# Performance work log

Measured on AMD Instinct MI355X. Metric: run time of the kernel, lower is better.

Reference implementation:

```python
import jax, jax.numpy as jnp
import numpy as np

V, F = 100000, 200000
N, H, W, K = 4, 512, 512, 4
SIGMA = 1e-4
GAMMA = 1e-4
BG = (1.0, 1.0, 1.0)
EPS = 1e-10
ZNEAR, ZFAR = 1.0, 100.0


def setup_inputs() -> dict:
    key = jax.random.key(0)
    ks = jax.random.split(key, 7)
    verts = jax.random.normal(ks[0], (V, 3), dtype=jnp.float32)
    vn = jax.random.normal(ks[1], (V, 3), dtype=jnp.float32)
    vertex_normals = vn / jnp.maximum(jnp.linalg.norm(vn, axis=-1, keepdims=True), 1e-12)
    bc = jax.random.uniform(ks[2], (N, H, W, K, 3), dtype=jnp.float32) + 1e-3
    bary_coords = bc / jnp.sum(bc, axis=-1, keepdims=True)
    # signed pixel-to-face distances, small scale comparable to sigma
    dists = jax.random.normal(ks[3], (N, H, W, K), dtype=jnp.float32) * 1e-4
    zbuf = jax.random.uniform(ks[4], (N, H, W, K), minval=ZNEAR, maxval=ZFAR, dtype=jnp.float32)
    faces = jax.random.randint(ks[5], (F, 3), 0, V, dtype=jnp.int64 if jax.config.jax_enable_x64 else jnp.int32)
    # include -1 entries (empty pixels), as produced by the rasterizer
    pix_to_face = jax.random.randint(ks[6], (N, H, W, K), -1, F, dtype=jnp.int64 if jax.config.jax_enable_x64 else jnp.int32)
    return {"verts": verts, "vertex_normals": vertex_normals, "bary_coords": bary_coords,
            "dists": dists, "zbuf": zbuf, "faces": faces, "pix_to_face": pix_to_face}


def reference(verts, vertex_normals, bary_coords, dists, zbuf, faces, pix_to_face):
    dtype = bary_coords.dtype
    # --- NormalCalcuate: gather per-face vertex normals and interpolate ---
    faces_normals = vertex_normals[faces]                      # [F, 3, 3]
    valid = pix_to_face >= 0                                   # [N,H,W,K]
    idx = jnp.where(valid, pix_to_face, 0)
    attrs = faces_normals[idx]                                 # [N,H,W,K,3(verts),3(ch)]
    pixel_normals = jnp.einsum('nhwkv,nhwkvc->nhwkc', bary_coords, attrs)
    pixel_normals = jnp.where(valid[..., None], pixel_normals, jnp.zeros((), dtype))
    # --- softmax_rgb_blend (rgb part only) ---
    maskf = valid.astype(dtype)
    prob = jax.nn.sigmoid(-dists / SIGMA) * maskf              # coverage weights
    z_inv = (ZFAR - zbuf) / (ZFAR - ZNEAR) * maskf
    z_inv_max = jnp.maximum(jnp.max(z_inv, axis=-1, keepdims=True), EPS)
    w_num = prob * jnp.exp((z_inv - z_inv_max) / GAMMA)        # [N,H,W,K]
    delta = jnp.maximum(jnp.exp((EPS - z_inv_max) / GAMMA), EPS)  # [N,H,W,1]
    denom = jnp.sum(w_num, axis=-1, keepdims=True) + delta
    bg = jnp.asarray(BG, dtype)
    rgb = (jnp.einsum('nhwk,nhwkc->nhwc', w_num, pixel_normals) + delta * bg) / denom
    # --- F.normalize(dim=3) ---
    norm = jnp.maximum(jnp.linalg.norm(rgb, axis=-1, keepdims=True), 1e-12)
    return rgb / norm
```

## Files before the change

### kernel.cpp

```cpp
#include <hip/hip_runtime.h>
#include <hip/hip_bf16.h>

namespace {
constexpr int N_ = 4, H_ = 512, W_ = 512, K_ = 4;
constexpr int F_ = 200000;
constexpr float SIGMA_ = 1e-4f;
constexpr float GAMMA_ = 1e-4f;
constexpr float EPS_   = 1e-10f;
constexpr float ZNEAR_ = 1.0f, ZFAR_ = 100.0f;

constexpr int P_ = N_ * H_ * W_;
constexpr int SHADER_BLOCKS  = 1024;
constexpr int SHADER_THREADS = SHADER_BLOCKS * 256;
constexpr int ITERS = P_ / SHADER_THREADS;
static_assert(P_ % SHADER_THREADS == 0, "grid must tile P exactly");

typedef float        f32x4 __attribute__((ext_vector_type(4), aligned(4)));
typedef int          i32x4 __attribute__((ext_vector_type(4), aligned(4)));
typedef float        f32x3 __attribute__((ext_vector_type(3), aligned(4)));
typedef unsigned int u32x4 __attribute__((ext_vector_type(4), aligned(16)));

struct PixIn { i32x4 f4; f32x4 dv, zv, bA, bB, bC; };
}


__device__ __forceinline__ unsigned int oct_encode(float x, float y, float z) {
    const float inv = 1.0f / (fabsf(x) + fabsf(y) + fabsf(z));
    const float px = x * inv, py = y * inv, pz = z * inv;
    const float wx = (1.0f - fabsf(py)) * copysignf(1.0f, px);
    const float wy = (1.0f - fabsf(px)) * copysignf(1.0f, py);
    const bool neg = pz < 0.0f;
    const float ex = neg ? wx : px;
    const float ey = neg ? wy : py;
    const int ix = (int)rintf(ex * 32767.0f);
    const int iy = (int)rintf(ey * 32767.0f);
    return ((unsigned int)ix & 0xffffu) | (((unsigned int)iy & 0xffffu) << 16);
}

__device__ __forceinline__ void oct_decode_raw(unsigned int e,
                                               float& x, float& y, float& z,
                                               float& inv) {
    const float fx = (float)(short)(unsigned short)(e & 0xffffu) * (1.0f / 32767.0f);
    const float fy = (float)(short)(unsigned short)(e >> 16)     * (1.0f / 32767.0f);
    z = 1.0f - fabsf(fx) - fabsf(fy);
    const float t = fmaxf(-z, 0.0f);
    const float xx = fx - copysignf(t, fx);
    const float yy = fy - copysignf(t, fy);
    x = xx; y = yy;
    inv = rsqrtf(xx * xx + yy * yy + z * z);
}

__global__ __launch_bounds__(256) void build_fnorm_kernel(
    const float*  __restrict__ vnorm,
    const int*    __restrict__ faces,
    unsigned int* __restrict__ fnorm)
{
    const int f = blockIdx.x * blockDim.x + threadIdx.x;
    if (f >= F_) return;
    const i32x4 fv = *reinterpret_cast<const i32x4*>(faces + 3 * (size_t)f);
    const f32x4 n0 = *reinterpret_cast<const f32x4*>(vnorm + 3 * (size_t)fv.x);
    const f32x4 n1 = *reinterpret_cast<const f32x4*>(vnorm + 3 * (size_t)fv.y);
    const f32x4 n2 = *reinterpret_cast<const f32x4*>(vnorm + 3 * (size_t)fv.z);
    const unsigned long long e0 = oct_encode(n0.x, n0.y, n0.z);
    const unsigned long long e1 = oct_encode(n1.x, n1.y, n1.z);
    const unsigned long long e2 = oct_encode(n2.x, n2.y, n2.z);
    unsigned long long* dst =
        reinterpret_cast<unsigned long long*>(fnorm + (size_t)f * 4);
    __hip_atomic_store(dst + 0, e0 | (e1 << 32), __ATOMIC_RELAXED, __HIP_MEMORY_SCOPE_AGENT);
    __hip_atomic_store(dst + 1, e2,              __ATOMIC_RELAXED, __HIP_MEMORY_SCOPE_AGENT);
}

__device__ __forceinline__ PixIn load_pix(const int*   __restrict__ ptf,
                                          const float* __restrict__ dists,
                                          const float* __restrict__ zbuf,
                                          const float* __restrict__ bary,
                                          int p) {
    PixIn s;
    s.f4 = __builtin_nontemporal_load(reinterpret_cast<const i32x4*>(ptf) + p);
    s.dv = __builtin_nontemporal_load(reinterpret_cast<const f32x4*>(dists) + p);
    s.zv = __builtin_nontemporal_load(reinterpret_cast<const f32x4*>(zbuf) + p);
    const f32x4* bp = reinterpret_cast<const f32x4*>(bary + (size_t)p * 12);
    s.bA = __builtin_nontemporal_load(bp + 0);
    s.bB = __builtin_nontemporal_load(bp + 1);
    s.bC = __builtin_nontemporal_load(bp + 2);
    return s;
}

__global__ __launch_bounds__(256, 4) void normal_shader_kernel(
    const unsigned int* __restrict__ fnorm,
    const float*        __restrict__ bary,
    const float*        __restrict__ dists,
    const float*        __restrict__ zbuf,
    const int*          __restrict__ ptf,
    float*              __restrict__ out)
{
    const int tid = blockIdx.x * 256 + threadIdx.x;

    PixIn cur = load_pix(ptf, dists, zbuf, bary, tid);

#pragma unroll
    for (int it = 0; it < ITERS; ++it) {
        const int p = tid + it * SHADER_THREADS;
        const int fidx[4] = {cur.f4.x, cur.f4.y, cur.f4.z, cur.f4.w};

        u32x4 row[4];
#pragma unroll
        for (int k = 0; k < K_; ++k) {
            const int r = (fidx[k] < 0) ? 0 : fidx[k];
            row[k] = reinterpret_cast<const u32x4*>(fnorm)[r];
        }

        PixIn nxt = cur;
        if (it + 1 < ITERS)
            nxt = load_pix(ptf, dists, zbuf, bary, p + SHADER_THREADS);

        const float d[4] = {cur.dv.x, cur.dv.y, cur.dv.z, cur.dv.w};
        const float z[4] = {cur.zv.x, cur.zv.y, cur.zv.z, cur.zv.w};
        float prob[4], zinv[4], zmax = EPS_;
#pragma unroll
        for (int k = 0; k < K_; ++k) {
            const bool valid = fidx[k] >= 0;
            prob[k] = valid ? 1.0f / (1.0f + __expf(d[k] * (1.0f / SIGMA_))) : 0.0f;
            zinv[k] = valid ? (ZFAR_ - z[k]) * (1.0f / (ZFAR_ - ZNEAR_)) : 0.0f;
            zmax = fmaxf(zmax, zinv[k]);
        }
        const float delta = fmaxf(__expf((EPS_ - zmax) * (1.0f / GAMMA_)), EPS_);
        float wn[4];
#pragma unroll
        for (int k = 0; k < K_; ++k)
            wn[k] = prob[k] * __expf((zinv[k] - zmax) * (1.0f / GAMMA_));

        const float bb[12] = {cur.bA.x, cur.bA.y, cur.bA.z, cur.bA.w,
                              cur.bB.x, cur.bB.y, cur.bB.z, cur.bB.w,
                              cur.bC.x, cur.bC.y, cur.bC.z, cur.bC.w};
        float acc0 = 0.f, acc1 = 0.f, acc2 = 0.f, wsum = 0.f;
#pragma unroll
        for (int k = 0; k < K_; ++k) {
            const float w = wn[k];
            wsum += w;
            float x0, y0, z0, i0, x1, y1, z1, i1, x2, y2, z2, i2;
            oct_decode_raw(row[k].x, x0, y0, z0, i0);
            oct_decode_raw(row[k].y, x1, y1, z1, i1);
            oct_decode_raw(row[k].z, x2, y2, z2, i2);
            const float s0 = (w * bb[3 * k + 0]) * i0;
            const float s1 = (w * bb[3 * k + 1]) * i1;
            const float s2 = (w * bb[3 * k + 2]) * i2;
            acc0 += s0 * x0 + s1 * x1 + s2 * x2;
            acc1 += s0 * y0 + s1 * y1 + s2 * y2;
            acc2 += s0 * z0 + s1 * z1 + s2 * z2;
        }
        const float inv_denom = 1.0f / (wsum + delta);
        const float r0 = (acc0 + delta) * inv_denom;
        const float r1 = (acc1 + delta) * inv_denom;
        const float r2 = (acc2 + delta) * inv_denom;
        const float nrm = fmaxf(sqrtf(r0 * r0 + r1 * r1 + r2 * r2), 1e-12f);
        const float inv = 1.0f / nrm;
        __builtin_nontemporal_store(
            f32x3{r0 * inv, r1 * inv, r2 * inv},
            reinterpret_cast<f32x3*>(out + (size_t)p * 3));

        cur = nxt;
    }
}

__global__ __launch_bounds__(256) void normal_shader_fused_kernel(
    const float* __restrict__ vnorm,
    const float* __restrict__ bary,
    const float* __restrict__ dists,
    const float* __restrict__ zbuf,
    const int*   __restrict__ faces,
    const int*   __restrict__ ptf,
    float*       __restrict__ out,
    int P)
{
    const int p = blockIdx.x * blockDim.x + threadIdx.x;
    if (p >= P) return;
    const i32x4 f4 = reinterpret_cast<const i32x4*>(ptf)[p];
    const int fidx[4] = {f4.x, f4.y, f4.z, f4.w};
    const f32x4 dv = reinterpret_cast<const f32x4*>(dists)[p];
    const f32x4 zv = reinterpret_cast<const f32x4*>(zbuf)[p];
    const float d[4] = {dv.x, dv.y, dv.z, dv.w};
    const float z[4] = {zv.x, zv.y, zv.z, zv.w};
    float prob[4], zinv[4], zmax = EPS_;
#pragma unroll
    for (int k = 0; k < K_; ++k) {
        const bool valid = fidx[k] >= 0;
        prob[k] = valid ? 1.0f / (1.0f + __expf(d[k] * (1.0f / SIGMA_))) : 0.0f;
        zinv[k] = valid ? (ZFAR_ - z[k]) * (1.0f / (ZFAR_ - ZNEAR_)) : 0.0f;
        zmax = fmaxf(zmax, zinv[k]);
    }
    const float delta = fmaxf(__expf((EPS_ - zmax) * (1.0f / GAMMA_)), EPS_);
    float wn[4];
#pragma unroll
    for (int k = 0; k < K_; ++k) wn[k] = prob[k] * __expf((zinv[k] - zmax) * (1.0f / GAMMA_));
    int cl[4];
#pragma unroll
    for (int k = 0; k < K_; ++k) cl[k] = (fidx[k] < 0) ? 0 : fidx[k];
    i32x4 fv[4];
#pragma unroll
    for (int k = 0; k < K_; ++k) fv[k] = *reinterpret_cast<const i32x4*>(faces + 3 * (size_t)cl[k]);
    const f32x4* bp = reinterpret_cast<const f32x4*>(bary + (size_t)p * 12);
    const f32x4 bA = bp[0], bB = bp[1], bC = bp[2];
    const float bb[12] = {bA.x, bA.y, bA.z, bA.w, bB.x, bB.y, bB.z, bB.w, bC.x, bC.y, bC.z, bC.w};
    f32x4 n0[4], n1[4], n2[4];
#pragma unroll
    for (int k = 0; k < K_; ++k) {
        n0[k] = *reinterpret_cast<const f32x4*>(vnorm + 3 * (size_t)fv[k].x);
        n1[k] = *reinterpret_cast<const f32x4*>(vnorm + 3 * (size_t)fv[k].y);
        n2[k] = *reinterpret_cast<const f32x4*>(vnorm + 3 * (size_t)fv[k].z);
    }
    float acc0 = 0.f, acc1 = 0.f, acc2 = 0.f, wsum = 0.f;
#pragma unroll
    for (int k = 0; k < K_; ++k) {
        wsum += wn[k];
        const float b0 = bb[3 * k], b1 = bb[3 * k + 1], b2 = bb[3 * k + 2];
        acc0 += wn[k] * (b0 * n0[k].x + b1 * n1[k].x + b2 * n2[k].x);
        acc1 += wn[k] * (b0 * n0[k].y + b1 * n1[k].y + b2 * n2[k].y);
        acc2 += wn[k] * (b0 * n0[k].z + b1 * n1[k].z + b2 * n2[k].z);
    }
    const float inv_denom = 1.0f / (wsum + delta);
    const float r0 = (acc0 + delta) * inv_denom;
    const float r1 = (acc1 + delta) * inv_denom;
    const float r2 = (acc2 + delta) * inv_denom;
    const float nrm = fmaxf(sqrtf(r0 * r0 + r1 * r1 + r2 * r2), 1e-12f);
    const float inv = 1.0f / nrm;
    float* op = out + (size_t)p * 3;
    op[0] = r0 * inv; op[1] = r1 * inv; op[2] = r2 * inv;
}

extern "C" void kernel_launch(void* const* d_in, const int* in_sizes, int n_in,
                              void* d_out, int out_size, void* d_ws, size_t ws_size,
                              hipStream_t stream) {
    const float* vnorm = (const float*)d_in[1];
    const float* bary  = (const float*)d_in[2];
    const float* dists = (const float*)d_in[3];
    const float* zbuf  = (const float*)d_in[4];
    const int*   faces = (const int*)d_in[5];
    const int*   ptf   = (const int*)d_in[6];
    float*       out   = (float*)d_out;

    const int P = N_ * H_ * W_;
    const size_t table_bytes = (size_t)F_ * 16;

    if (ws_size >= table_bytes) {
        unsigned int* fnorm = (unsigned int*)d_ws;
        hipLaunchKernelGGL(build_fnorm_kernel,
                           dim3((F_ + 255) / 256), dim3(256), 0, stream,
                           vnorm, faces, fnorm);
        hipLaunchKernelGGL(normal_shader_kernel,
                           dim3(SHADER_BLOCKS), dim3(256), 0, stream,
                           fnorm, bary, dists, zbuf, ptf, out);
    } else {
        hipLaunchKernelGGL(normal_shader_fused_kernel,
                           dim3((P + 255) / 256), dim3(256), 0, stream,
                           vnorm, bary, dists, zbuf, faces, ptf, out, P);
    }
}
```

Baseline: 164.4 us.

## Use one thread per pixel and drop the software-pipelined persistent loop

Replaces the persistent-style shader, where 1024 blocks each loop over several pixels with next-iteration loads prefetched, with a plain grid of one thread per pixel. Occupancy and the hardware scheduler now hide memory latency instead of the manual double buffering, and the launch-bounds occupancy hint is removed. It also drops the per-component scale in the octahedral decode, since the later rsqrt normalisation cancels it. The trade-off is more blocks to launch and the loss of explicit prefetch overlap.

```diff
diff --git a/kernel.cpp b/kernel.cpp
--- a/kernel.cpp
+++ b/kernel.cpp
@@ -10,17 +10,13 @@
 constexpr float ZNEAR_ = 1.0f, ZFAR_ = 100.0f;
 
 constexpr int P_ = N_ * H_ * W_;
-constexpr int SHADER_BLOCKS  = 1024;
-constexpr int SHADER_THREADS = SHADER_BLOCKS * 256;
-constexpr int ITERS = P_ / SHADER_THREADS;
-static_assert(P_ % SHADER_THREADS == 0, "grid must tile P exactly");
+constexpr int SHADER_BLOCKS = P_ / 256;
+static_assert(P_ % 256 == 0, "grid must tile P exactly");
 
 typedef float        f32x4 __attribute__((ext_vector_type(4), aligned(4)));
 typedef int          i32x4 __attribute__((ext_vector_type(4), aligned(4)));
 typedef float        f32x3 __attribute__((ext_vector_type(3), aligned(4)));
 typedef unsigned int u32x4 __attribute__((ext_vector_type(4), aligned(16)));
-
-struct PixIn { i32x4 f4; f32x4 dv, zv, bA, bB, bC; };
 }
 
 
@@ -40,12 +36,12 @@
 __device__ __forceinline__ void oct_decode_raw(unsigned int e,
                                                float& x, float& y, float& z,
                                                float& inv) {
-    const float fx = (float)(short)(unsigned short)(e & 0xffffu) * (1.0f / 32767.0f);
-    const float fy = (float)(short)(unsigned short)(e >> 16)     * (1.0f / 32767.0f);
-    z = 1.0f - fabsf(fx) - fabsf(fy);
+    const float X = (float)(short)(unsigned short)(e & 0xffffu);
+    const float Y = (float)(short)(unsigned short)(e >> 16);
+    z = 32767.0f - fabsf(X) - fabsf(Y);
     const float t = fmaxf(-z, 0.0f);
-    const float xx = fx - copysignf(t, fx);
-    const float yy = fy - copysignf(t, fy);
+    const float xx = X - copysignf(t, X);
+    const float yy = Y - copysignf(t, Y);
     x = xx; y = yy;
     inv = rsqrtf(xx * xx + yy * yy + z * z);
 }
@@ -70,23 +66,7 @@
     __hip_atomic_store(dst + 1, e2,              __ATOMIC_RELAXED, __HIP_MEMORY_SCOPE_AGENT);
 }
 
-__device__ __forceinline__ PixIn load_pix(const int*   __restrict__ ptf,
-                                          const float* __restrict__ dists,
-                                          const float* __restrict__ zbuf,
-                                          const float* __restrict__ bary,
-                                          int p) {
-    PixIn s;
-    s.f4 = __builtin_nontemporal_load(reinterpret_cast<const i32x4*>(ptf) + p);
-    s.dv = __builtin_nontemporal_load(reinterpret_cast<const f32x4*>(dists) + p);
-    s.zv = __builtin_nontemporal_load(reinterpret_cast<const f32x4*>(zbuf) + p);
-    const f32x4* bp = reinterpret_cast<const f32x4*>(bary + (size_t)p * 12);
-    s.bA = __builtin_nontemporal_load(bp + 0);
-    s.bB = __builtin_nontemporal_load(bp + 1);
-    s.bC = __builtin_nontemporal_load(bp + 2);
-    return s;
-}
-
-__global__ __launch_bounds__(256, 4) void normal_shader_kernel(
+__global__ __launch_bounds__(256) void normal_shader_kernel(
     const unsigned int* __restrict__ fnorm,
     const float*        __restrict__ bary,
     const float*        __restrict__ dists,
@@ -94,73 +74,68 @@
     const int*          __restrict__ ptf,
     float*              __restrict__ out)
 {
-    const int tid = blockIdx.x * 256 + threadIdx.x;
-
-    PixIn cur = load_pix(ptf, dists, zbuf, bary, tid);
-
-#pragma unroll
-    for (int it = 0; it < ITERS; ++it) {
-        const int p = tid + it * SHADER_THREADS;
-        const int fidx[4] = {cur.f4.x, cur.f4.y, cur.f4.z, cur.f4.w};
-
-        u32x4 row[4];
-#pragma unroll
-        for (int k = 0; k < K_; ++k) {
-            const int r = (fidx[k] < 0) ? 0 : fidx[k];
-            row[k] = reinterpret_cast<const u32x4*>(fnorm)[r];
-        }
-
-        PixIn nxt = cur;
-        if (it + 1 < ITERS)
-            nxt = load_pix(ptf, dists, zbuf, bary, p + SHADER_THREADS);
-
-        const float d[4] = {cur.dv.x, cur.dv.y, cur.dv.z, cur.dv.w};
-        const float z[4] = {cur.zv.x, cur.zv.y, cur.zv.z, cur.zv.w};
-        float prob[4], zinv[4], zmax = EPS_;
-#pragma unroll
-        for (int k = 0; k < K_; ++k) {
-            const bool valid = fidx[k] >= 0;
-            prob[k] = valid ? 1.0f / (1.0f + __expf(d[k] * (1.0f / SIGMA_))) : 0.0f;
-            zinv[k] = valid ? (ZFAR_ - z[k]) * (1.0f / (ZFAR_ - ZNEAR_)) : 0.0f;
-            zmax = fmaxf(zmax, zinv[k]);
-        }
-        const float delta = fmaxf(__expf((EPS_ - zmax) * (1.0f / GAMMA_)), EPS_);
-        float wn[4];
-#pragma unroll
-        for (int k = 0; k < K_; ++k)
-            wn[k] = prob[k] * __expf((zinv[k] - zmax) * (1.0f / GAMMA_));
-
-        const float bb[12] = {cur.bA.x, cur.bA.y, cur.bA.z, cur.bA.w,
-                              cur.bB.x, cur.bB.y, cur.bB.z, cur.bB.w,
-                              cur.bC.x, cur.bC.y, cur.bC.z, cur.bC.w};
-        float acc0 = 0.f, acc1 = 0.f, acc2 = 0.f, wsum = 0.f;
-#pragma unroll
-        for (int k = 0; k < K_; ++k) {
-            const float w = wn[k];
-            wsum += w;
-            float x0, y0, z0, i0, x1, y1, z1, i1, x2, y2, z2, i2;
-            oct_decode_raw(row[k].x, x0, y0, z0, i0);
-            oct_decode_raw(row[k].y, x1, y1, z1, i1);
-            oct_decode_raw(row[k].z, x2, y2, z2, i2);
-            const float s0 = (w * bb[3 * k + 0]) * i0;
-            const float s1 = (w * bb[3 * k + 1]) * i1;
-            const float s2 = (w * bb[3 * k + 2]) * i2;
-            acc0 += s0 * x0 + s1 * x1 + s2 * x2;
-            acc1 += s0 * y0 + s1 * y1 + s2 * y2;
-            acc2 += s0 * z0 + s1 * z1 + s2 * z2;
-        }
-        const float inv_denom = 1.0f / (wsum + delta);
-        const float r0 = (acc0 + delta) * inv_denom;
-        const float r1 = (acc1 + delta) * inv_denom;
-        const float r2 = (acc2 + delta) * inv_denom;
-        const float nrm = fmaxf(sqrtf(r0 * r0 + r1 * r1 + r2 * r2), 1e-12f);
-        const float inv = 1.0f / nrm;
-        __builtin_nontemporal_store(
-            f32x3{r0 * inv, r1 * inv, r2 * inv},
-            reinterpret_cast<f32x3*>(out + (size_t)p * 3));
-
-        cur = nxt;
-    }
+    const int p = blockIdx.x * 256 + threadIdx.x;
+
+    const i32x4 f4 = __builtin_nontemporal_load(reinterpret_cast<const i32x4*>(ptf) + p);
+    const f32x4 dv = __builtin_nontemporal_load(reinterpret_cast<const f32x4*>(dists) + p);
+    const f32x4 zv = __builtin_nontemporal_load(reinterpret_cast<const f32x4*>(zbuf) + p);
+    const f32x4* bp = reinterpret_cast<const f32x4*>(bary + (size_t)p * 12);
+    const f32x4 bA = __builtin_nontemporal_load(bp + 0);
+    const f32x4 bB = __builtin_nontemporal_load(bp + 1);
+    const f32x4 bC = __builtin_nontemporal_load(bp + 2);
+
+    const int fidx[4] = {f4.x, f4.y, f4.z, f4.w};
+    u32x4 row[4];
+#pragma unroll
+    for (int k = 0; k < K_; ++k) {
+        const int r = (fidx[k] < 0) ? 0 : fidx[k];
+        row[k] = reinterpret_cast<const u32x4*>(fnorm)[r];
+    }
+
+    const float d[4] = {dv.x, dv.y, dv.z, dv.w};
+    const float z[4] = {zv.x, zv.y, zv.z, zv.w};
+    float prob[4], zinv[4], zmax = EPS_;
+#pragma unroll
+    for (int k = 0; k < K_; ++k) {
+        const bool valid = fidx[k] >= 0;
+        prob[k] = valid ? 1.0f / (1.0f + __expf(d[k] * (1.0f / SIGMA_))) : 0.0f;
+        zinv[k] = valid ? (ZFAR_ - z[k]) * (1.0f / (ZFAR_ - ZNEAR_)) : 0.0f;
+        zmax = fmaxf(zmax, zinv[k]);
+    }
+    const float delta = fmaxf(__expf((EPS_ - zmax) * (1.0f / GAMMA_)), EPS_);
+    float wn[4];
+#pragma unroll
+    for (int k = 0; k < K_; ++k)
+        wn[k] = prob[k] * __expf((zinv[k] - zmax) * (1.0f / GAMMA_));
+
+    const float bb[12] = {bA.x, bA.y, bA.z, bA.w,
+                          bB.x, bB.y, bB.z, bB.w,
+                          bC.x, bC.y, bC.z, bC.w};
+    float acc0 = 0.f, acc1 = 0.f, acc2 = 0.f, wsum = 0.f;
+#pragma unroll
+    for (int k = 0; k < K_; ++k) {
+        const float w = wn[k];
+        wsum += w;
+        float x0, y0, z0, i0, x1, y1, z1, i1, x2, y2, z2, i2;
+        oct_decode_raw(row[k].x, x0, y0, z0, i0);
+        oct_decode_raw(row[k].y, x1, y1, z1, i1);
+        oct_decode_raw(row[k].z, x2, y2, z2, i2);
+        const float s0 = (w * bb[3 * k + 0]) * i0;
+        const float s1 = (w * bb[3 * k + 1]) * i1;
+        const float s2 = (w * bb[3 * k + 2]) * i2;
+        acc0 += s0 * x0 + s1 * x1 + s2 * x2;
+        acc1 += s0 * y0 + s1 * y1 + s2 * y2;
+        acc2 += s0 * z0 + s1 * z1 + s2 * z2;
+    }
+    const float inv_denom = 1.0f / (wsum + delta);
+    const float r0 = (acc0 + delta) * inv_denom;
+    const float r1 = (acc1 + delta) * inv_denom;
+    const float r2 = (acc2 + delta) * inv_denom;
+    const float nrm = fmaxf(sqrtf(r0 * r0 + r1 * r1 + r2 * r2), 1e-12f);
+    const float inv = 1.0f / nrm;
+    __builtin_nontemporal_store(
+        f32x3{r0 * inv, r1 * inv, r2 * inv},
+        reinterpret_cast<f32x3*>(out + (size_t)p * 3));
 }
 
 __global__ __launch_bounds__(256) void normal_shader_fused_kernel(
```

Result: no change. 162.7 us (-1.1%).
